# Performance work log

Measured on AMD Instinct MI355X. Metric: run time of the kernel, lower is better.

Reference implementation:

```python
import jax, jax.numpy as jnp
import numpy as np
from functools import partial

T = 16  # number of ODE time steps (h = 1/T)


def _q(x0, xt, t):
    """Nadaraya-Watson Gaussian RBF retrieval.
    x0: (B, d) memory bank, xt: (N, d) queries, t: scalar time.
    Returns qt: (N, d).
    Original torch code subtracts the *global* min of zz before exp;
    that constant cancels in the row-wise normalization, so this is
    exactly a softmax over the bank dimension of -0.5*||z||^2.
    """
    sigma_t = t
    alpha_t = 1.0 - t
    # (N, B, d) diff tensor -- the dominant memory traffic
    z = (xt[:, None, :] - alpha_t * x0[None, :, :]) / sigma_t
    zz = jnp.sum(z * z, axis=-1)                 # (N, B)
    wt = jax.nn.softmax(-0.5 * zz, axis=-1)      # (N, B)
    return wt @ x0                               # (N, d)


def _G(x0, xt, t):
    return (xt - _q(x0, xt, t)) / t


def setup_inputs() -> dict:
    key = jax.random.key(0)
    k1, k2 = jax.random.split(key)
    x1 = jax.random.normal(k1, (2048, 8), dtype=jnp.float32)   # (N, d) Gaussian states at t=1
    x0 = jax.random.normal(k2, (4096, 8), dtype=jnp.float32)   # (B, d) memory bank / data batch
    return {"x1": x1, "x0": x0}


def reference(x1, x0):
    h = 1.0 / T
    G1 = _G(x0, x1, 1.0)
    # Heun (trapezoidal predictor-corrector) integration from t=1 down to t=h.
    # t after step i (0-based) is 1 - h*(i+1); always > 0 for i < T-1.
    t_vals = 1.0 - h * (jnp.arange(1, T, dtype=jnp.float32))   # (T-1,)

    def step(carry, t):
        xt, G1 = carry
        G2 = _G(x0, xt - G1 * h, t)
        xt = xt - (G1 + G2) * (h * 0.5)
        return (xt, G2), None

    (xt, _), _ = jax.lax.scan(step, (x1, G1), t_vals)
    return xt  # (N, d)
```

## Files before the change

### kernel.cpp

```cpp
#include <hip/hip_runtime.h>


#define NQ     2048
#define NB     4096
#define DD     8
#define TSTEPS 16
#define BLOCK  512
#define QPB    8

#if defined(__has_builtin)
#if __has_builtin(__builtin_amdgcn_exp2f)
#define EXP2(x) __builtin_amdgcn_exp2f(x)
#endif
#endif
#ifndef EXP2
#define EXP2(x) exp2f(x)
#endif

__device__ __forceinline__ void eval_G(const float4* __restrict__ lds_lo,
                                       const float4* __restrict__ lds_hi,
                                       const float* x, float t, int lane,
                                       float* Gout) {
    const float alpha = 1.0f - t;
    const float c0 = -0.72134752044448170f / (t * t);

    float m = -1e30f;
    float s = 0.0f;
    float q[DD];
#pragma unroll
    for (int j = 0; j < DD; ++j) q[j] = 0.0f;

#pragma unroll 2
    for (int k = 0; k < NB / 64; k += 4) {
        float4 lo[4], hi[4];
        float  l[4];
#pragma unroll
        for (int e = 0; e < 4; ++e) {
            const int b = lane + (k + e) * 64;
            lo[e] = lds_lo[b];
            hi[e] = lds_hi[b];
            float z, zz;
            z = fmaf(-alpha, lo[e].x, x[0]); zz = z * z;
            z = fmaf(-alpha, lo[e].y, x[1]); zz = fmaf(z, z, zz);
            z = fmaf(-alpha, lo[e].z, x[2]); zz = fmaf(z, z, zz);
            z = fmaf(-alpha, lo[e].w, x[3]); zz = fmaf(z, z, zz);
            z = fmaf(-alpha, hi[e].x, x[4]); zz = fmaf(z, z, zz);
            z = fmaf(-alpha, hi[e].y, x[5]); zz = fmaf(z, z, zz);
            z = fmaf(-alpha, hi[e].z, x[6]); zz = fmaf(z, z, zz);
            z = fmaf(-alpha, hi[e].w, x[7]); zz = fmaf(z, z, zz);
            l[e] = zz * c0;
        }
        const float bm = fmaxf(fmaxf(l[0], l[1]), fmaxf(l[2], l[3]));
        if (__any(bm > m + 40.0f)) {
            const float mn = fmaxf(m, bm);
            const float c = EXP2(m - mn);
            s *= c;
#pragma unroll
            for (int j = 0; j < DD; ++j) q[j] *= c;
            m = mn;
        }
#pragma unroll
        for (int e = 0; e < 4; ++e) {
            const float w = EXP2(l[e] - m);
            s += w;
            q[0] = fmaf(w, lo[e].x, q[0]);
            q[1] = fmaf(w, lo[e].y, q[1]);
            q[2] = fmaf(w, lo[e].z, q[2]);
            q[3] = fmaf(w, lo[e].w, q[3]);
            q[4] = fmaf(w, hi[e].x, q[4]);
            q[5] = fmaf(w, hi[e].y, q[5]);
            q[6] = fmaf(w, hi[e].z, q[6]);
            q[7] = fmaf(w, hi[e].w, q[7]);
        }
    }

    float mw = m;
#pragma unroll
    for (int off = 32; off >= 1; off >>= 1)
        mw = fmaxf(mw, __shfl_xor(mw, off));
    const float c = EXP2(m - mw);
    s *= c;
#pragma unroll
    for (int j = 0; j < DD; ++j) q[j] *= c;
#pragma unroll
    for (int off = 32; off >= 1; off >>= 1) {
        s += __shfl_xor(s, off);
#pragma unroll
        for (int j = 0; j < DD; ++j) q[j] += __shfl_xor(q[j], off);
    }

    const float inv = 1.0f / s;
#pragma unroll
    for (int j = 0; j < DD; ++j)
        Gout[j] = (x[j] - q[j] * inv) / t;
}

__global__ __launch_bounds__(BLOCK, 2) void flow_ode_kernel(
        const float* __restrict__ x1,
        const float* __restrict__ x0,
        float* __restrict__ out) {
    __shared__ float4 lds_lo[NB];
    __shared__ float4 lds_hi[NB];

    const int tid = threadIdx.x;
    for (int b = tid; b < NB; b += BLOCK) {
        const float4* p = reinterpret_cast<const float4*>(x0) + 2 * b;
        lds_lo[b] = p[0];
        lds_hi[b] = p[1];
    }
    __syncthreads();

    const int wave = tid >> 6;
    const int lane = tid & 63;
    const int n = blockIdx.x * QPB + wave;
    if (n >= NQ) return;

    float xt[DD], G1[DD], G2[DD];
#pragma unroll
    for (int j = 0; j < DD; ++j) xt[j] = x1[n * DD + j];

    eval_G(lds_lo, lds_hi, xt, 1.0f, lane, G1);

    const float h = 0.0625f;
    for (int i = 1; i < TSTEPS; ++i) {
        const float t = 1.0f - h * (float)i;
        float xe[DD];
#pragma unroll
        for (int j = 0; j < DD; ++j) xe[j] = fmaf(-h, G1[j], xt[j]);
        eval_G(lds_lo, lds_hi, xe, t, lane, G2);
#pragma unroll
        for (int j = 0; j < DD; ++j) {
            xt[j] = fmaf(-0.03125f, G1[j] + G2[j], xt[j]);
            G1[j] = G2[j];
        }
    }

    if (lane == 0) {
        float4 a, b;
        a.x = xt[0]; a.y = xt[1]; a.z = xt[2]; a.w = xt[3];
        b.x = xt[4]; b.y = xt[5]; b.z = xt[6]; b.w = xt[7];
        float4* o = reinterpret_cast<float4*>(out + n * DD);
        o[0] = a;
        o[1] = b;
    }
}

extern "C" void kernel_launch(void* const* d_in, const int* in_sizes, int n_in,
                              void* d_out, int out_size, void* d_ws, size_t ws_size,
                              hipStream_t stream) {
    const float* x1 = (const float*)d_in[0];
    const float* x0 = (const float*)d_in[1];
    float* out = (float*)d_out;

    const int nblocks = NQ / QPB;
    flow_ode_kernel<<<nblocks, BLOCK, 0, stream>>>(x1, x0, out);
}
```

Baseline: 178.5 us.

## Share LDS bank loads across query pairs and skip the t=1 evaluation

Each wave now processes two queries over half of the memory bank, so every LDS load of a bank row is reused for two distance computations. Partial softmax states from paired waves are merged through shared memory, with block-wide barriers added each step. The first G evaluation at t=1 is replaced by the analytic bank mean, computed while staging x0 into LDS, removing one full pass. The running max is tracked on squared distances to trim per-element arithmetic, at the cost of more registers and extra synchronisation.

```diff
diff --git a/kernel.cpp b/kernel.cpp
--- a/kernel.cpp
+++ b/kernel.cpp
@@ -3,10 +3,8 @@
 
 #define NQ     2048
 #define NB     4096
-#define DD     8
 #define TSTEPS 16
 #define BLOCK  512
-#define QPB    8
 
 #if defined(__has_builtin)
 #if __has_builtin(__builtin_amdgcn_exp2f)
@@ -17,131 +15,222 @@
 #define EXP2(x) exp2f(x)
 #endif
 
-__device__ __forceinline__ void eval_G(const float4* __restrict__ lds_lo,
-                                       const float4* __restrict__ lds_hi,
-                                       const float* x, float t, int lane,
-                                       float* Gout) {
-    const float alpha = 1.0f - t;
-    const float c0 = -0.72134752044448170f / (t * t);
-
-    float m = -1e30f;
-    float s = 0.0f;
-    float q[DD];
-#pragma unroll
-    for (int j = 0; j < DD; ++j) q[j] = 0.0f;
+__device__ __forceinline__ void eval_pair(
+        const float4* __restrict__ lds_lo,
+        const float4* __restrict__ lds_hi,
+        float (*mrg)[2][12],
+        const float (&xq)[2][8], float t, int lane, int h, int w,
+        float (&Gout)[2][8])
+{
+    const float c0      = -0.72134752044448170f / (t * t);
+    const float alpha   = 1.0f - t;
+    const float thr_off = 40.0f / c0;
+    float mz[2] = {3.0e38f, 3.0e38f};
+    float th[2] = {3.0e38f, 3.0e38f};
+    float t0[2] = {0.0f, 0.0f};
+    float s[2]  = {0.0f, 0.0f};
+    float q[2][8];
+#pragma unroll
+    for (int qq = 0; qq < 2; ++qq)
+#pragma unroll
+        for (int j = 0; j < 8; ++j) q[qq][j] = 0.0f;
+
+    const int b0 = lane + h * 2048;
 
 #pragma unroll 2
-    for (int k = 0; k < NB / 64; k += 4) {
+    for (int g = 0; g < 8; ++g) {
         float4 lo[4], hi[4];
-        float  l[4];
+        float  zz[2][4];
 #pragma unroll
         for (int e = 0; e < 4; ++e) {
-            const int b = lane + (k + e) * 64;
+            const int b = b0 + g * 256 + e * 64;
             lo[e] = lds_lo[b];
             hi[e] = lds_hi[b];
-            float z, zz;
-            z = fmaf(-alpha, lo[e].x, x[0]); zz = z * z;
-            z = fmaf(-alpha, lo[e].y, x[1]); zz = fmaf(z, z, zz);
-            z = fmaf(-alpha, lo[e].z, x[2]); zz = fmaf(z, z, zz);
-            z = fmaf(-alpha, lo[e].w, x[3]); zz = fmaf(z, z, zz);
-            z = fmaf(-alpha, hi[e].x, x[4]); zz = fmaf(z, z, zz);
-            z = fmaf(-alpha, hi[e].y, x[5]); zz = fmaf(z, z, zz);
-            z = fmaf(-alpha, hi[e].z, x[6]); zz = fmaf(z, z, zz);
-            z = fmaf(-alpha, hi[e].w, x[7]); zz = fmaf(z, z, zz);
-            l[e] = zz * c0;
-        }
-        const float bm = fmaxf(fmaxf(l[0], l[1]), fmaxf(l[2], l[3]));
-        if (__any(bm > m + 40.0f)) {
-            const float mn = fmaxf(m, bm);
-            const float c = EXP2(m - mn);
-            s *= c;
-#pragma unroll
-            for (int j = 0; j < DD; ++j) q[j] *= c;
-            m = mn;
-        }
-#pragma unroll
-        for (int e = 0; e < 4; ++e) {
-            const float w = EXP2(l[e] - m);
-            s += w;
-            q[0] = fmaf(w, lo[e].x, q[0]);
-            q[1] = fmaf(w, lo[e].y, q[1]);
-            q[2] = fmaf(w, lo[e].z, q[2]);
-            q[3] = fmaf(w, lo[e].w, q[3]);
-            q[4] = fmaf(w, hi[e].x, q[4]);
-            q[5] = fmaf(w, hi[e].y, q[5]);
-            q[6] = fmaf(w, hi[e].z, q[6]);
-            q[7] = fmaf(w, hi[e].w, q[7]);
-        }
-    }
-
-    float mw = m;
-#pragma unroll
-    for (int off = 32; off >= 1; off >>= 1)
-        mw = fmaxf(mw, __shfl_xor(mw, off));
-    const float c = EXP2(m - mw);
-    s *= c;
-#pragma unroll
-    for (int j = 0; j < DD; ++j) q[j] *= c;
-#pragma unroll
-    for (int off = 32; off >= 1; off >>= 1) {
-        s += __shfl_xor(s, off);
-#pragma unroll
-        for (int j = 0; j < DD; ++j) q[j] += __shfl_xor(q[j], off);
-    }
-
-    const float inv = 1.0f / s;
-#pragma unroll
-    for (int j = 0; j < DD; ++j)
-        Gout[j] = (x[j] - q[j] * inv) / t;
+#pragma unroll
+            for (int qq = 0; qq < 2; ++qq) {
+                float z, acc;
+                z = fmaf(-alpha, lo[e].x, xq[qq][0]); acc = z * z;
+                z = fmaf(-alpha, lo[e].y, xq[qq][1]); acc = fmaf(z, z, acc);
+                z = fmaf(-alpha, lo[e].z, xq[qq][2]); acc = fmaf(z, z, acc);
+                z = fmaf(-alpha, lo[e].w, xq[qq][3]); acc = fmaf(z, z, acc);
+                z = fmaf(-alpha, hi[e].x, xq[qq][4]); acc = fmaf(z, z, acc);
+                z = fmaf(-alpha, hi[e].y, xq[qq][5]); acc = fmaf(z, z, acc);
+                z = fmaf(-alpha, hi[e].z, xq[qq][6]); acc = fmaf(z, z, acc);
+                z = fmaf(-alpha, hi[e].w, xq[qq][7]); acc = fmaf(z, z, acc);
+                zz[qq][e] = acc;
+            }
+        }
+#pragma unroll
+        for (int qq = 0; qq < 2; ++qq) {
+            const float bz = fminf(fminf(zz[qq][0], zz[qq][1]),
+                                   fminf(zz[qq][2], zz[qq][3]));
+            if (__any(bz < th[qq])) {
+                const float mzn = fminf(mz[qq], bz);
+                const float c = EXP2(c0 * (mz[qq] - mzn));
+                s[qq] *= c;
+#pragma unroll
+                for (int j = 0; j < 8; ++j) q[qq][j] *= c;
+                mz[qq] = mzn;
+                th[qq] = mzn + thr_off;
+                t0[qq] = -c0 * mzn;
+            }
+#pragma unroll
+            for (int e = 0; e < 4; ++e) {
+                const float wgt = EXP2(fmaf(c0, zz[qq][e], t0[qq]));
+                s[qq] += wgt;
+                q[qq][0] = fmaf(wgt, lo[e].x, q[qq][0]);
+                q[qq][1] = fmaf(wgt, lo[e].y, q[qq][1]);
+                q[qq][2] = fmaf(wgt, lo[e].z, q[qq][2]);
+                q[qq][3] = fmaf(wgt, lo[e].w, q[qq][3]);
+                q[qq][4] = fmaf(wgt, hi[e].x, q[qq][4]);
+                q[qq][5] = fmaf(wgt, hi[e].y, q[qq][5]);
+                q[qq][6] = fmaf(wgt, hi[e].z, q[qq][6]);
+                q[qq][7] = fmaf(wgt, hi[e].w, q[qq][7]);
+            }
+        }
+    }
+
+#pragma unroll
+    for (int qq = 0; qq < 2; ++qq) {
+        float mw = mz[qq];
+#pragma unroll
+        for (int off = 32; off >= 1; off >>= 1)
+            mw = fminf(mw, __shfl_xor(mw, off));
+        const float c = EXP2(c0 * (mz[qq] - mw));
+        s[qq] *= c;
+#pragma unroll
+        for (int j = 0; j < 8; ++j) q[qq][j] *= c;
+        mz[qq] = mw;
+#pragma unroll
+        for (int off = 32; off >= 1; off >>= 1) {
+            s[qq] += __shfl_xor(s[qq], off);
+#pragma unroll
+            for (int j = 0; j < 8; ++j) q[qq][j] += __shfl_xor(q[qq][j], off);
+        }
+    }
+
+    if (lane == 0) {
+#pragma unroll
+        for (int qq = 0; qq < 2; ++qq) {
+            float* p = mrg[w][qq];
+            p[0] = mz[qq];
+            p[1] = s[qq];
+#pragma unroll
+            for (int j = 0; j < 8; ++j) p[2 + j] = q[qq][j];
+        }
+    }
+    __syncthreads();
+    const int pw = w ^ 1;
+    const float invT = 1.0f / t;
+#pragma unroll
+    for (int qq = 0; qq < 2; ++qq) {
+        const float* p = mrg[pw][qq];
+        const float mzb = p[0], sb = p[1];
+        const float M  = fminf(mz[qq], mzb);
+        const float ca = EXP2(c0 * (mz[qq] - M));
+        const float cb = EXP2(c0 * (mzb  - M));
+        const float S  = ca * s[qq] + cb * sb;
+        const float invS = 1.0f / S;
+#pragma unroll
+        for (int j = 0; j < 8; ++j) {
+            const float Q = ca * q[qq][j] + cb * p[2 + j];
+            Gout[qq][j] = fmaf(-Q, invS, xq[qq][j]) * invT;
+        }
+    }
+    __syncthreads();
 }
 
 __global__ __launch_bounds__(BLOCK, 2) void flow_ode_kernel(
         const float* __restrict__ x1,
         const float* __restrict__ x0,
-        float* __restrict__ out) {
+        float* __restrict__ out)
+{
     __shared__ float4 lds_lo[NB];
     __shared__ float4 lds_hi[NB];
-
-    const int tid = threadIdx.x;
-    for (int b = tid; b < NB; b += BLOCK) {
+    __shared__ float  mrg[8][2][12];
+
+    const int tid  = threadIdx.x;
+    const int w    = tid >> 6;
+    const int lane = tid & 63;
+
+    float sm[8];
+#pragma unroll
+    for (int j = 0; j < 8; ++j) sm[j] = 0.0f;
+#pragma unroll
+    for (int i = 0; i < NB / BLOCK; ++i) {
+        const int b = tid + i * BLOCK;
         const float4* p = reinterpret_cast<const float4*>(x0) + 2 * b;
-        lds_lo[b] = p[0];
-        lds_hi[b] = p[1];
-    }
-    __syncthreads();
-
-    const int wave = tid >> 6;
-    const int lane = tid & 63;
-    const int n = blockIdx.x * QPB + wave;
-    if (n >= NQ) return;
-
-    float xt[DD], G1[DD], G2[DD];
-#pragma unroll
-    for (int j = 0; j < DD; ++j) xt[j] = x1[n * DD + j];
-
-    eval_G(lds_lo, lds_hi, xt, 1.0f, lane, G1);
-
-    const float h = 0.0625f;
+        const float4 lo = p[0], hi = p[1];
+        lds_lo[b] = lo;
+        lds_hi[b] = hi;
+        sm[0] += lo.x; sm[1] += lo.y; sm[2] += lo.z; sm[3] += lo.w;
+        sm[4] += hi.x; sm[5] += hi.y; sm[6] += hi.z; sm[7] += hi.w;
+    }
+#pragma unroll
+    for (int off = 32; off >= 1; off >>= 1)
+#pragma unroll
+        for (int j = 0; j < 8; ++j) sm[j] += __shfl_xor(sm[j], off);
+    if (lane == 0) {
+#pragma unroll
+        for (int j = 0; j < 8; ++j) mrg[w][0][j] = sm[j];
+    }
+    __syncthreads();
+    float mean[8];
+#pragma unroll
+    for (int j = 0; j < 8; ++j) {
+        float acc = 0.0f;
+#pragma unroll
+        for (int wv = 0; wv < 8; ++wv) acc += mrg[wv][0][j];
+        mean[j] = acc * (1.0f / (float)NB);
+    }
+    __syncthreads();
+
+    const int h     = w & 1;
+    const int pair  = w >> 1;
+    const int qbase = blockIdx.x * 8 + pair * 2;
+
+    float xt[2][8], G1[2][8];
+#pragma unroll
+    for (int qq = 0; qq < 2; ++qq) {
+        const float4* p = reinterpret_cast<const float4*>(x1) + 2 * (qbase + qq);
+        const float4 a = p[0], b4 = p[1];
+        xt[qq][0] = a.x;  xt[qq][1] = a.y;  xt[qq][2] = a.z;  xt[qq][3] = a.w;
+        xt[qq][4] = b4.x; xt[qq][5] = b4.y; xt[qq][6] = b4.z; xt[qq][7] = b4.w;
+    }
+#pragma unroll
+    for (int qq = 0; qq < 2; ++qq)
+#pragma unroll
+        for (int j = 0; j < 8; ++j) G1[qq][j] = xt[qq][j] - mean[j];
+
+    const float hstep = 0.0625f;
     for (int i = 1; i < TSTEPS; ++i) {
-        const float t = 1.0f - h * (float)i;
-        float xe[DD];
-#pragma unroll
-        for (int j = 0; j < DD; ++j) xe[j] = fmaf(-h, G1[j], xt[j]);
-        eval_G(lds_lo, lds_hi, xe, t, lane, G2);
-#pragma unroll
-        for (int j = 0; j < DD; ++j) {
-            xt[j] = fmaf(-0.03125f, G1[j] + G2[j], xt[j]);
-            G1[j] = G2[j];
-        }
-    }
-
-    if (lane == 0) {
-        float4 a, b;
-        a.x = xt[0]; a.y = xt[1]; a.z = xt[2]; a.w = xt[3];
-        b.x = xt[4]; b.y = xt[5]; b.z = xt[6]; b.w = xt[7];
-        float4* o = reinterpret_cast<float4*>(out + n * DD);
-        o[0] = a;
-        o[1] = b;
+        const float t = 1.0f - hstep * (float)i;
+        float xe[2][8], G2[2][8];
+#pragma unroll
+        for (int qq = 0; qq < 2; ++qq)
+#pragma unroll
+            for (int j = 0; j < 8; ++j)
+                xe[qq][j] = fmaf(-hstep, G1[qq][j], xt[qq][j]);
+        eval_pair(lds_lo, lds_hi, mrg, xe, t, lane, h, w, G2);
+#pragma unroll
+        for (int qq = 0; qq < 2; ++qq)
+#pragma unroll
+            for (int j = 0; j < 8; ++j) {
+                xt[qq][j] = fmaf(-0.03125f, G1[qq][j] + G2[qq][j], xt[qq][j]);
+                G1[qq][j] = G2[qq][j];
+            }
+    }
+
+    if (h == 0 && lane == 0) {
+#pragma unroll
+        for (int qq = 0; qq < 2; ++qq) {
+            float4 a, b4;
+            a.x  = xt[qq][0]; a.y  = xt[qq][1]; a.z  = xt[qq][2]; a.w  = xt[qq][3];
+            b4.x = xt[qq][4]; b4.y = xt[qq][5]; b4.z = xt[qq][6]; b4.w = xt[qq][7];
+            float4* o = reinterpret_cast<float4*>(out + (qbase + qq) * 8);
+            o[0] = a;
+            o[1] = b4;
+        }
     }
 }
 
@@ -152,6 +241,5 @@
     const float* x0 = (const float*)d_in[1];
     float* out = (float*)d_out;
 
-    const int nblocks = NQ / QPB;
-    flow_ode_kernel<<<nblocks, BLOCK, 0, stream>>>(x1, x0, out);
+    flow_ode_kernel<<<NQ / 8, BLOCK, 0, stream>>>(x1, x0, out);
 }
```

After: 185.9 us. 4.1% more time.
